# Performance work log

Hardware: AMD Instinct MI355X
Metric: run time of the kernel (lower is better)

## Reference

```python
import jax, jax.numpy as jnp
import numpy as np

B = 32768   # batch
F = 32      # per-node feature dim
H = 256     # hidden width
M = 4       # modules per node
OUT = 8     # final output dim
INIT_W = 0.003
B_INIT = 0.1


def _lin(k, din, dout):
    # fanin_init-style uniform weights, bias filled with 0.1 (hidden layers)
    s = 1.0 / np.sqrt(din)
    W = jax.random.uniform(k, (M, din, dout), jnp.float32, -s, s)
    b = jnp.full((M, dout), B_INIT, jnp.float32)
    return W, b


def setup_inputs() -> dict:
    key = jax.random.key(0)
    ks = jax.random.split(key, 16)
    feats = jax.random.normal(ks[0], (B, 4 * F), jnp.float32)
    idx = jax.random.randint(ks[1], (B, 4), 0, M)
    onehots = jax.nn.one_hot(idx, M, dtype=jnp.float32).reshape(B, 4 * M)
    input_val = jnp.concatenate([feats, onehots], axis=1)  # [B,144]

    W00, b00 = _lin(ks[2], F, H)        # node0 post layer 0
    W01, b01 = _lin(ks[3], H, H)        # node0 post layer 1
    Wpre1, bpre1 = _lin(ks[4], F, H)    # node1 pre
    Wpost1, bpost1 = _lin(ks[5], 2 * H, H)  # node1 interface (prev 256 + own 256)
    Wpre2, bpre2 = _lin(ks[6], F, H)
    Wpost2, bpost2 = _lin(ks[7], 2 * H, H)
    Wpre3, bpre3 = _lin(ks[8], F, H)
    Wpost3, bpost3 = _lin(ks[9], 2 * H, H)
    # final output layer: uniform(-init_w, init_w) for W and b, identity act
    Wfin3 = jax.random.uniform(ks[10], (M, H, OUT), jnp.float32, -INIT_W, INIT_W)
    bfin3 = jax.random.uniform(ks[11], (M, OUT), jnp.float32, -INIT_W, INIT_W)
    return dict(input_val=input_val,
                W00=W00, b00=b00, W01=W01, b01=b01,
                Wpre1=Wpre1, bpre1=bpre1, Wpost1=Wpost1, bpost1=bpost1,
                Wpre2=Wpre2, bpre2=bpre2, Wpost2=Wpost2, bpost2=bpost2,
                Wpre3=Wpre3, bpre3=bpre3, Wpost3=Wpost3, bpost3=bpost3,
                Wfin3=Wfin3, bfin3=bfin3)


def _select(h, onehot):
    # per-row pick of the assigned module's output: [B,M,D],[B,M] -> [B,D]
    return jnp.einsum('bmo,bm->bo', h, onehot)


def reference(input_val, W00, b00, W01, b01,
              Wpre1, bpre1, Wpost1, bpost1,
              Wpre2, bpre2, Wpost2, bpost2,
              Wpre3, bpre3, Wpost3, bpost3,
              Wfin3, bfin3):
    feat = lambda j: input_val[:, j * F:(j + 1) * F]
    oh = lambda j: input_val[:, 4 * F + j * M: 4 * F + (j + 1) * M]

    # node 0: two hidden layers, module-dispatched (dense-all-modules + one-hot combine)
    h = jax.nn.relu(jnp.einsum('bi,mio->bmo', feat(0), W00) + b00)
    h = jax.nn.relu(jnp.einsum('bmi,mio->bmo', h, W01) + b01)
    x = _select(h, oh(0))  # [B,H]

    def node(x_prev, fj, ohj, Wpre, bpre, Wpost, bpost):
        hp = jax.nn.relu(jnp.einsum('bi,mio->bmo', fj, Wpre) + bpre)
        # interface layer consumes concat([x_prev, hp]); split the weight to
        # avoid materializing [B,M,2H]
        hq = jax.nn.relu(jnp.einsum('bi,mio->bmo', x_prev, Wpost[:, :H, :])
                         + jnp.einsum('bmi,mio->bmo', hp, Wpost[:, H:, :])
                         + bpost)
        return hq  # [B,M,H]

    x = _select(node(x, feat(1), oh(1), Wpre1, bpre1, Wpost1, bpost1), oh(1))
    x = _select(node(x, feat(2), oh(2), Wpre2, bpre2, Wpost2, bpost2), oh(2))

    h3 = node(x, feat(3), oh(3), Wpre3, bpre3, Wpost3, bpost3)  # [B,M,H]
    out = jnp.einsum('bmi,mio->bmo', h3, Wfin3) + bfin3          # final linear, identity act
    return _select(out, oh(3))  # [B,OUT]
```

## Files before the change

kernel.cpp:

```cpp
#include <hip/hip_runtime.h>

#define NB 32768
#define MAXTILE 768
#define ROWS 64
#define NT 4
#define XHS 536

typedef short s8v __attribute__((ext_vector_type(8)));
typedef short s4v __attribute__((ext_vector_type(4)));
typedef float f4v __attribute__((ext_vector_type(4)));
typedef unsigned short u16;
typedef unsigned short u16x4 __attribute__((ext_vector_type(4)));
typedef unsigned int u32;
typedef unsigned char u8;

__device__ __forceinline__ float bf2f(u16 u) { return __uint_as_float(((u32)u) << 16); }
__device__ __forceinline__ u16 f2bf(float f) {
    u32 x = __float_as_uint(f);
    x += 0x7FFFu + ((x >> 16) & 1u);
    return (u16)(x >> 16);
}
__device__ __forceinline__ s8v ld8(const u16* p) { return *reinterpret_cast<const s8v*>(p); }

#define MFMA16(a, b, c) __builtin_amdgcn_mfma_f32_16x16x32_bf16((a), (b), (c), 0, 0, 0)

template <int N> struct IC { static constexpr int v = N; };

__device__ __forceinline__ void detect_flag(const void* input, int tid, int* shflag)
{
    if (tid < 64) {
        u32 w = ((const u32*)input)[tid];
        u32 h0 = w & 0xFFFFu;
        u32 e0 = (h0 >> 7) & 0xFFu;
        bool plaus = (h0 == 0u) || (e0 >= 96u && e0 <= 143u);
        unsigned long long m = __ballot(plaus);
        if (tid == 0) *shflag = (__popcll(m) >= 48) ? 1 : 0;
    }
}

struct RepArgs {
    const void* W01; const void* Wp[3]; const void* pre[4]; const void* fin;
    const void* bias[9];
    u16 *rPre, *rW01, *rWp[3], *rFin, *cbias;
};

__global__ __launch_bounds__(256) void prepA_kernel(const void* __restrict__ inputv,
                                                    int* __restrict__ gcnt,
                                                    int* __restrict__ perm2,
                                                    RepArgs R)
{
    __shared__ int lcnt[256];
    __shared__ int sBase[256];
    __shared__ u16 T[8192];
    __shared__ int shmisc;
    int tid = threadIdx.x;
    int b = blockIdx.x;
    detect_flag(inputv, tid, &shmisc);
    __syncthreads();
    int flag = shmisc;

    if (b < 128) {
        lcnt[tid] = 0;
        __syncthreads();
        int row = (b << 8) + tid;
        const u32* in32 = (const u32*)inputv;
        const u16* in16 = (const u16*)inputv;
        int key = 0;
        if (flag) {
#pragma unroll
            for (int j = 0; j < 4; j++) {
                u16x4 v = *(const u16x4*)(in16 + row * 144 + 128 + j * 4);
                int m = v[1] ? 1 : (v[2] ? 2 : (v[3] ? 3 : 0));
                key |= m << (j << 1);
            }
        } else {
#pragma unroll
            for (int j = 0; j < 4; j++) {
                const u32* p = in32 + row * 144 + 128 + j * 4;
                u32 v1 = p[1], v2 = p[2], v3 = p[3];
                int m = v1 ? 1 : (v2 ? 2 : (v3 ? 3 : 0));
                key |= m << (j << 1);
            }
        }
        int loc = atomicAdd(&lcnt[key], 1);
        __syncthreads();
        int c = lcnt[tid];
        sBase[tid] = c ? atomicAdd(&gcnt[tid], c) : 0;
        __syncthreads();
        int slot = sBase[key] + loc;
        if (slot < 512) perm2[(key << 9) + slot] = row;
        return;
    }

    int rb = b - 128;
    const void* src = nullptr; u16* dst = nullptr; int K = 0, k0 = 0, mrow = 0;
    if (rb < 32) {
        int m = rb >> 3, s = rb & 7;
        src = R.W01; dst = R.rW01 + (m * 8 + s) * 8192; K = 256; k0 = s * 32; mrow = m;
    } else if (rb < 224) {
        int idx = rb - 32, mat = idx >> 6, r = idx & 63, m = r >> 4, s = r & 15;
        src = R.Wp[mat]; dst = R.rWp[mat] + (m * 16 + s) * 8192; K = 512; k0 = s * 32; mrow = m;
    } else if (rb < 240) {
        int idx = rb - 224, mat = idx >> 2, m = idx & 3;
        src = R.pre[mat]; dst = R.rPre + (mat * 4 + m) * 8192; K = 32; k0 = 0; mrow = m;
    } else if (rb < 244) {
        int m = rb - 240;
        const u16* s16 = (const u16*)R.fin;
        const float* s32 = (const float*)R.fin;
        for (int i = tid; i < 2048; i += 256) {
            int si = (m * 256 + (i >> 3)) * 8 + (i & 7);
            T[i] = flag ? s16[si] : f2bf(s32[si]);
        }
        __syncthreads();
        u16* d = R.rFin + m * 4096;
        for (int i = tid; i < 4096; i += 256) {
            int s = i >> 9, lane = (i >> 3) & 63, j = i & 7;
            int q = lane >> 4, l16 = lane & 15;
            int k = s * 32 + q * 8 + j;
            d[i] = (l16 < 8) ? T[k * 8 + l16] : (u16)0;
        }
        return;
    } else {
        const int sz[9] = {1024,1024,1024,1024,1024,1024,1024,1024,32};
        const int of[9] = {0,1024,2048,3072,4096,5120,6144,7168,8192};
        for (int i = tid; i < 8224; i += 256) {
            int t = i, e = 0;
            while (t >= sz[e]) { t -= sz[e]; e++; }
            R.cbias[of[e] + t] = flag ? ((const u16*)R.bias[e])[t]
                                      : f2bf(((const float*)R.bias[e])[t]);
        }
        return;
    }
    const u16* s16 = (const u16*)src;
    const float* s32 = (const float*)src;
    for (int i = tid; i < 8192; i += 256) {
        int k = i >> 8, n = i & 255;
        int srcIdx = (mrow * K + k0 + k) * 256 + n;
        T[i] = flag ? s16[srcIdx] : f2bf(s32[srcIdx]);
    }
    __syncthreads();
    for (int i = tid; i < 8192; i += 256) {
        int mt = i >> 9, lane = (i >> 3) & 63, j = i & 7;
        int k = ((lane >> 4) << 3) + j, n = (mt << 4) + (lane & 15);
        dst[i] = T[(k << 8) + n];
    }
}

struct MainP { const u16 *rPre, *rW01, *rWp1, *rWp2, *rWp3, *rFin, *cbias; };

__global__ __launch_bounds__(512, 4) void main_kernel(
    const void* __restrict__ inRaw,
    const int* __restrict__ gcnt, const int* __restrict__ perm2,
    MainP P, void* __restrict__ outp)
{
    __shared__ __align__(16) u16 xh[ROWS * XHS];
    __shared__ int rowids[ROWS];
    __shared__ int shflag;
    __shared__ int sScan[256];
    __shared__ int sMeta[3];

    int tid = threadIdx.x;
    int lane = tid & 63, w = tid >> 6, quad = lane >> 4, l16 = lane & 15;

    int b = blockIdx.x;
    int t = ((b & 7) * (MAXTILE / 8)) + (b >> 3);

    detect_flag(inRaw, tid, &shflag);

    int myTiles = 0, myTot = 0;
    if (tid < 256) {
        myTot = gcnt[tid];
        myTiles = (myTot + ROWS - 1) >> 6;
        sScan[tid] = myTiles;
    }
    __syncthreads();
    for (int off = 1; off < 256; off <<= 1) {
        int v = (tid >= off && tid < 256) ? sScan[tid - off] : 0;
        __syncthreads();
        if (tid < 256) sScan[tid] += v;
        __syncthreads();
    }
    if (tid < 256 && myTiles) {
        int tb = sScan[tid] - myTiles;
        if (t >= tb && t < sScan[tid]) {
            sMeta[0] = tid;
            sMeta[1] = t - tb;
            sMeta[2] = myTot;
        }
    }
    __syncthreads();
    int ttot = sScan[255];
    if (t >= ttot) return;
    int key = sMeta[0], tau = sMeta[1], tot = sMeta[2];
    int cntIn = tot - tau * ROWS; if (cntIn > ROWS) cntIn = ROWS;
    if (tid < ROWS) {
        int g = tid < cntIn ? tid : cntIn - 1;
        rowids[tid] = perm2[(key << 9) + tau * ROWS + g];
    }
    __syncthreads();

    int flag = shflag;
    int rows_[NT];
#pragma unroll
    for (int nt = 0; nt < NT; nt++) rows_[nt] = rowids[nt * 16 + l16];

    const u16* in16 = (const u16*)inRaw;
    const float* in32 = (const float*)inRaw;
    int mt0 = w << 1, mt1 = mt0 + 1;

    f4v acc0[NT], acc1[NT];

    f4v raw0[NT], raw1[NT];
    auto issue_fb = [&](int node) {
#pragma unroll
        for (int nt = 0; nt < NT; nt++) {
            int off = rows_[nt] * 144 + (node << 5) + (quad << 3);
            if (flag) {
                raw0[nt] = *(const f4v*)(in16 + off);
            } else {
                raw0[nt] = *(const f4v*)(in32 + off);
                raw1[nt] = *(const f4v*)(in32 + off + 4);
            }
        }
    };
    auto conv_fb = [&](int nt) -> s8v {
        if (flag) return *(s8v*)&raw0[nt];
        s8v r;
#pragma unroll
        for (int j = 0; j < 4; j++) {
            r[j]     = (short)f2bf(raw0[nt][j]);
            r[4 + j] = (short)f2bf(raw1[nt][j]);
        }
        return r;
    };

    auto gemm_run = [&](auto nc, const u16* Ab, int ks0, int nextNode) {
        constexpr int N = decltype(nc)::v;
        constexpr int D = 4;
        const u16* base0 = Ab + mt0 * 512 + lane * 8;
        const u16* base1 = Ab + mt1 * 512 + lane * 8;
        s8v A0[D], A1[D];
#pragma unroll
        for (int d = 0; d < D && d < N; d++) {
            A0[d] = ld8(base0 + d * 8192);
            A1[d] = ld8(base1 + d * 8192);
        }
        if (nextNode >= 0) issue_fb(nextNode);
        __syncthreads();
        __builtin_amdgcn_s_setprio(1);
#pragma unroll
        for (int s = 0; s < N; s++) {
            s8v c0 = A0[s % D], c1 = A1[s % D];
            if (s + D < N) {
                A0[s % D] = ld8(base0 + (s + D) * 8192);
                A1[s % D] = ld8(base1 + (s + D) * 8192);
            }
#pragma unroll
            for (int nt = 0; nt < NT; nt++) {
                s8v B = ld8(&xh[(nt * 16 + l16) * XHS + (ks0 + s) * 32 + quad * 8]);
                acc0[nt] = MFMA16(c0, B, acc0[nt]);
                acc1[nt] = MFMA16(c1, B, acc1[nt]);
            }
        }
        __builtin_amdgcn_s_setprio(0);
    };

    issue_fb(0);
    for (int node = 0; node < 4; node++) {
        int m = (key >> (node << 1)) & 3;

        s8v fb[NT];
#pragma unroll
        for (int nt = 0; nt < NT; nt++) fb[nt] = conv_fb(nt);

        const u16* preB = P.rPre + ((node << 2) + m) * 8192;
#pragma unroll
        for (int ci = 0; ci < 2; ci++) {
            int mt = mt0 + ci;
            s8v a = ld8(preB + mt * 512 + lane * 8);
            u16x4 bv = *(const u16x4*)(P.cbias + node * 2048 + m * 256 + mt * 16 + quad * 4);
            f4v bias;
#pragma unroll
            for (int r = 0; r < 4; r++) bias[r] = bf2f(bv[r]);
#pragma unroll
            for (int nt = 0; nt < NT; nt++) {
                f4v c = MFMA16(a, fb[nt], bias);
                s4v p;
#pragma unroll
                for (int r = 0; r < 4; r++) { float v = c[r] > 0.f ? c[r] : 0.f; p[r] = (short)f2bf(v); }
                *(s4v*)&xh[(nt * 16 + l16) * XHS + 256 + mt * 16 + quad * 4] = p;
            }
        }

        {
            u16x4 b0 = *(const u16x4*)(P.cbias + node * 2048 + 1024 + m * 256 + mt0 * 16 + quad * 4);
            u16x4 b1 = *(const u16x4*)(P.cbias + node * 2048 + 1024 + m * 256 + mt1 * 16 + quad * 4);
            f4v f0, f1;
#pragma unroll
            for (int r = 0; r < 4; r++) { f0[r] = bf2f(b0[r]); f1[r] = bf2f(b1[r]); }
#pragma unroll
            for (int nt = 0; nt < NT; nt++) { acc0[nt] = f0; acc1[nt] = f1; }
        }

        if (node == 0) gemm_run(IC<8>{},  P.rW01 + m * 8 * 8192, 8, 1);
        else {
            const u16* WB = (node == 1 ? P.rWp1 : (node == 2 ? P.rWp2 : P.rWp3)) + m * 16 * 8192;
            gemm_run(IC<16>{}, WB, 0, node < 3 ? node + 1 : -1);
        }
        __syncthreads();

#pragma unroll
        for (int ci = 0; ci < 2; ci++) {
            int mt = mt0 + ci;
#pragma unroll
            for (int nt = 0; nt < NT; nt++) {
                f4v a = ci ? acc1[nt] : acc0[nt];
                s4v p;
#pragma unroll
                for (int r = 0; r < 4; r++) { float v = a[r] > 0.f ? a[r] : 0.f; p[r] = (short)f2bf(v); }
                *(s4v*)&xh[(nt * 16 + l16) * XHS + mt * 16 + quad * 4] = p;
            }
        }
    }
    __syncthreads();

    if (w < NT) {
        int m3 = (key >> 6) & 3;
        f4v c;
#pragma unroll
        for (int r = 0; r < 4; r++)
            c[r] = (quad < 2) ? bf2f(P.cbias[8192 + m3 * 8 + quad * 4 + r]) : 0.f;
#pragma unroll
        for (int s = 0; s < 8; s++) {
            s8v A = ld8(P.rFin + m3 * 4096 + s * 512 + lane * 8);
            s8v B = ld8(&xh[(w * 16 + l16) * XHS + s * 32 + quad * 8]);
            c = MFMA16(A, B, c);
        }
        int bidx = w * 16 + l16;
        if (quad < 2 && bidx < cntIn) {
            int row = rowids[bidx];
            if (flag) {
                s4v p;
#pragma unroll
                for (int r = 0; r < 4; r++) p[r] = (short)f2bf(c[r]);
                *(s4v*)((u16*)outp + row * 8 + quad * 4) = p;
            } else {
                *(f4v*)((float*)outp + row * 8 + quad * 4) = c;
            }
        }
    }
}

extern "C" void kernel_launch(void* const* d_in, const int* in_sizes, int n_in,
                              void* d_out, int out_size, void* d_ws, size_t ws_size,
                              hipStream_t stream)
{
    (void)in_sizes; (void)n_in; (void)out_size;
    const void* input  = d_in[0];
    const void* W00    = d_in[1];
    const void* b00    = d_in[2];
    const void* W01    = d_in[3];
    const void* b01    = d_in[4];
    const void* Wpre1  = d_in[5];
    const void* bpre1  = d_in[6];
    const void* Wpost1 = d_in[7];
    const void* bpost1 = d_in[8];
    const void* Wpre2  = d_in[9];
    const void* bpre2  = d_in[10];
    const void* Wpost2 = d_in[11];
    const void* bpost2 = d_in[12];
    const void* Wpre3  = d_in[13];
    const void* bpre3  = d_in[14];
    const void* Wpost3 = d_in[15];
    const void* bpost3 = d_in[16];
    const void* Wfin   = d_in[17];
    const void* bfin   = d_in[18];

    char* base = (char*)d_ws;
    size_t off = 0;
    auto alloc = [&](size_t bytes) -> char* {
        char* p = base + off;
        off += (bytes + 255) & ~(size_t)255;
        return p;
    };
    int*  gcnt      = (int*)alloc(256 * 4);
    int*  perm2     = (int*)alloc(256 * 512 * 4);
    u16*  cbias    = (u16*)alloc(8224 * 2);
    u16*  rPre     = (u16*)alloc(131072 * 2);
    u16*  rW01     = (u16*)alloc(262144 * 2);
    u16*  rWp1     = (u16*)alloc(524288 * 2);
    u16*  rWp2     = (u16*)alloc(524288 * 2);
    u16*  rWp3     = (u16*)alloc(524288 * 2);
    u16*  rFin     = (u16*)alloc(16384 * 2);
    if (off > ws_size) return;

    RepArgs R;
    R.W01 = W01; R.Wp[0] = Wpost1; R.Wp[1] = Wpost2; R.Wp[2] = Wpost3;
    R.pre[0] = W00; R.pre[1] = Wpre1; R.pre[2] = Wpre2; R.pre[3] = Wpre3;
    R.fin = Wfin;
    R.bias[0] = b00;   R.bias[1] = b01;
    R.bias[2] = bpre1; R.bias[3] = bpost1;
    R.bias[4] = bpre2; R.bias[5] = bpost2;
    R.bias[6] = bpre3; R.bias[7] = bpost3;
    R.bias[8] = bfin;
    R.rPre = rPre; R.rW01 = rW01;
    R.rWp[0] = rWp1; R.rWp[1] = rWp2; R.rWp[2] = rWp3;
    R.rFin = rFin; R.cbias = cbias;

    hipMemsetAsync(gcnt, 0, 256 * 4, stream);
    prepA_kernel<<<373, 256, 0, stream>>>(input, gcnt, perm2, R);

    MainP P;
    P.rPre = rPre; P.rW01 = rW01; P.rWp1 = rWp1; P.rWp2 = rWp2; P.rWp3 = rWp3;
    P.rFin = rFin; P.cbias = cbias;
    main_kernel<<<MAXTILE, 512, 0, stream>>>(input, gcnt, perm2, P, d_out);
}
```

Baseline: 225.7 us.

## Replace LDS tile scan with wave shuffle scan, drop feature prefetch, deepen weight prefetch

Replaces the 256-entry shared-memory Hillis-Steele scan, which needed many block barriers, with a single-wave shuffle scan over int4-loaded group counts, to cut per-block setup overhead. It removes the cross-node prefetch of per-node input features and loads them synchronously at the top of each node, freeing registers. It raises the weight-fragment prefetch depth from 4 to 6 for the 16-step GEMMs. Feature load latency is now exposed at each node start, and the deeper prefetch raises register pressure.

```diff
diff --git a/kernel.cpp b/kernel.cpp
--- a/kernel.cpp
+++ b/kernel.cpp
@@ -156,8 +156,7 @@
     __shared__ __align__(16) u16 xh[ROWS * XHS];
     __shared__ int rowids[ROWS];
     __shared__ int shflag;
-    __shared__ int sScan[256];
-    __shared__ int sMeta[3];
+    __shared__ int sMeta[4];
 
     int tid = threadIdx.x;
     int lane = tid & 63, w = tid >> 6, quad = lane >> 4, l16 = lane & 15;
@@ -167,30 +166,32 @@
 
     detect_flag(inRaw, tid, &shflag);
 
-    int myTiles = 0, myTot = 0;
-    if (tid < 256) {
-        myTot = gcnt[tid];
-        myTiles = (myTot + ROWS - 1) >> 6;
-        sScan[tid] = myTiles;
+    if (tid < 64) {
+        int4 g = *(const int4*)(gcnt + tid * 4);
+        int tot4[4] = {g.x, g.y, g.z, g.w};
+        int tiles4[4], lsum = 0;
+#pragma unroll
+        for (int j = 0; j < 4; j++) { tiles4[j] = (tot4[j] + 63) >> 6; lsum += tiles4[j]; }
+        int pre = lsum;
+#pragma unroll
+        for (int off = 1; off < 64; off <<= 1) {
+            int v = __shfl_up(pre, off, 64);
+            if (tid >= off) pre += v;
+        }
+        int run = pre - lsum;
+#pragma unroll
+        for (int j = 0; j < 4; j++) {
+            if (t >= run && t < run + tiles4[j]) {
+                sMeta[0] = tid * 4 + j;
+                sMeta[1] = t - run;
+                sMeta[2] = tot4[j];
+            }
+            run += tiles4[j];
+        }
+        if (tid == 63) sMeta[3] = pre;
     }
     __syncthreads();
-    for (int off = 1; off < 256; off <<= 1) {
-        int v = (tid >= off && tid < 256) ? sScan[tid - off] : 0;
-        __syncthreads();
-        if (tid < 256) sScan[tid] += v;
-        __syncthreads();
-    }
-    if (tid < 256 && myTiles) {
-        int tb = sScan[tid] - myTiles;
-        if (t >= tb && t < sScan[tid]) {
-            sMeta[0] = tid;
-            sMeta[1] = t - tb;
-            sMeta[2] = myTot;
-        }
-    }
-    __syncthreads();
-    int ttot = sScan[255];
-    if (t >= ttot) return;
+    if (t >= sMeta[3]) return;
     int key = sMeta[0], tau = sMeta[1], tot = sMeta[2];
     int cntIn = tot - tau * ROWS; if (cntIn > ROWS) cntIn = ROWS;
     if (tid < ROWS) {
@@ -210,33 +211,9 @@
 
     f4v acc0[NT], acc1[NT];
 
-    f4v raw0[NT], raw1[NT];
-    auto issue_fb = [&](int node) {
-#pragma unroll
-        for (int nt = 0; nt < NT; nt++) {
-            int off = rows_[nt] * 144 + (node << 5) + (quad << 3);
-            if (flag) {
-                raw0[nt] = *(const f4v*)(in16 + off);
-            } else {
-                raw0[nt] = *(const f4v*)(in32 + off);
-                raw1[nt] = *(const f4v*)(in32 + off + 4);
-            }
-        }
-    };
-    auto conv_fb = [&](int nt) -> s8v {
-        if (flag) return *(s8v*)&raw0[nt];
-        s8v r;
-#pragma unroll
-        for (int j = 0; j < 4; j++) {
-            r[j]     = (short)f2bf(raw0[nt][j]);
-            r[4 + j] = (short)f2bf(raw1[nt][j]);
-        }
-        return r;
-    };
-
-    auto gemm_run = [&](auto nc, const u16* Ab, int ks0, int nextNode) {
+    auto gemm_run = [&](auto nc, const u16* Ab, int ks0) {
         constexpr int N = decltype(nc)::v;
-        constexpr int D = 4;
+        constexpr int D = (N > 8) ? 6 : 4;
         const u16* base0 = Ab + mt0 * 512 + lane * 8;
         const u16* base1 = Ab + mt1 * 512 + lane * 8;
         s8v A0[D], A1[D];
@@ -245,7 +222,6 @@
             A0[d] = ld8(base0 + d * 8192);
             A1[d] = ld8(base1 + d * 8192);
         }
-        if (nextNode >= 0) issue_fb(nextNode);
         __syncthreads();
         __builtin_amdgcn_s_setprio(1);
 #pragma unroll
@@ -265,13 +241,23 @@
         __builtin_amdgcn_s_setprio(0);
     };
 
-    issue_fb(0);
     for (int node = 0; node < 4; node++) {
         int m = (key >> (node << 1)) & 3;
 
         s8v fb[NT];
 #pragma unroll
-        for (int nt = 0; nt < NT; nt++) fb[nt] = conv_fb(nt);
+        for (int nt = 0; nt < NT; nt++) {
+            int off = rows_[nt] * 144 + (node << 5) + (quad << 3);
+            if (flag) fb[nt] = ld8(in16 + off);
+            else {
+                f4v f0 = *(const f4v*)(in32 + off);
+                f4v f1 = *(const f4v*)(in32 + off + 4);
+                s8v r;
+#pragma unroll
+                for (int j = 0; j < 4; j++) { r[j] = (short)f2bf(f0[j]); r[4 + j] = (short)f2bf(f1[j]); }
+                fb[nt] = r;
+            }
+        }
 
         const u16* preB = P.rPre + ((node << 2) + m) * 8192;
 #pragma unroll
@@ -302,10 +288,10 @@
             for (int nt = 0; nt < NT; nt++) { acc0[nt] = f0; acc1[nt] = f1; }
         }
 
-        if (node == 0) gemm_run(IC<8>{},  P.rW01 + m * 8 * 8192, 8, 1);
+        if (node == 0) gemm_run(IC<8>{},  P.rW01 + m * 8 * 8192, 8);
         else {
             const u16* WB = (node == 1 ? P.rWp1 : (node == 2 ? P.rWp2 : P.rWp3)) + m * 16 * 8192;
-            gemm_run(IC<16>{}, WB, 0, node < 3 ? node + 1 : -1);
+            gemm_run(IC<16>{}, WB, 0);
         }
         __syncthreads();
 
```

New measurement: 191.3 us. 1.18x faster.
